# Performance work log

Hardware: AMD Instinct MI355X
Metric: run time of the kernel (lower is better)

## Reference

```python
import jax, jax.numpy as jnp
import numpy as np

N, L, H, K, T = 768, 8, 64, 4, 3

def _mlp2(x, w1, b1, w2, b2):
    # Linear -> ReLU -> Linear -> ReLU (matches nn.Sequential in q/k/v MLPs)
    return jax.nn.relu(jax.nn.relu(x @ w1 + b1) @ w2 + b2)

def setup_inputs() -> dict:
    key = jax.random.key(0)
    ks = jax.random.split(key, 20)
    s = 1.0 / np.sqrt(H)
    def lin(k, din, dout):
        return jax.random.uniform(k, (din, dout), jnp.float32, -s, s)
    def bias(k, dout):
        return jax.random.uniform(k, (dout,), jnp.float32, -s, s)
    inp = {
        "h": jax.random.normal(ks[0], (N, L, H), jnp.float32),
        "coord": jax.random.normal(ks[1], (N, L, K, T), jnp.float32),
        "wq1": lin(ks[2], H, H), "bq1": bias(ks[3], H),
        "wq2": lin(ks[4], H, H), "bq2": bias(ks[5], H),
        "wk1": lin(ks[6], H, H), "bk1": bias(ks[7], H),
        "wk2": lin(ks[8], H, H), "bk2": bias(ks[9], H),
        "wv1": lin(ks[10], H, H), "bv1": bias(ks[11], H),
        "wv2": lin(ks[12], H, H), "bv2": bias(ks[13], H),
        "wc1": lin(ks[14], H, H), "bc1": bias(ks[15], H),
        # final coord layer: Linear(H, 4, bias=False), xavier gain=0.001
        "wc2": jax.random.normal(ks[16], (H, K), jnp.float32) * 0.001,
    }
    return inp

def reference(h, coord, wq1, bq1, wq2, bq2, wk1, bk1, wk2, bk2,
              wv1, bv1, wv2, bv2, wc1, bc1, wc2):
    q = _mlp2(h, wq1, bq1, wq2, bq2)          # [N, L, H]
    k = _mlp2(h, wk1, bk1, wk2, bk2)          # [N, L, H]
    v = _mlp2(h, wv1, bv1, wv2, bv2)          # [N, L, H]
    # scores[i, j, l] = <q_i, k_j> per frame l; softmax over neighbor axis j (dim=1)
    scores = jnp.einsum('ilh,jlh->ijl', q, k)
    alpha = jax.nn.softmax(scores, axis=1)     # [N, N, L]
    h_agg = jnp.einsum('ijl,jlh->ilh', alpha, v)
    cmv = jax.nn.relu(v @ wc1 + bc1) @ wc2     # coord_mlp(v): [N, L, 4]
    coord_diff = coord[:, None] - coord[None]  # [N, N, L, 4, 3]
    x_agg = jnp.einsum('ijlkt,ijl,jlk->ilkt', coord_diff, alpha, cmv)
    return (h + h_agg, coord + x_agg)
```

## Files before the change

### kernel.cpp

```cpp
#include <hip/hip_runtime.h>
#include <hip/hip_bf16.h>

#define NN 768
#define LL 8
#define HH 64
#define IT 16
#define ABP 776
#define XST 80
#define WST 72

typedef __attribute__((ext_vector_type(8))) short bf16x8;
typedef __attribute__((ext_vector_type(4))) float f32x4;

__device__ __forceinline__ short f2bf(float x) {
    union { __hip_bfloat16 h; short s; } u;
    u.h = __float2bfloat16(x);
    return u.s;
}

__device__ __forceinline__ bf16x8 pack8(float4 lo, float4 hi) {
    bf16x8 r;
    r[0] = f2bf(lo.x); r[1] = f2bf(lo.y); r[2] = f2bf(lo.z); r[3] = f2bf(lo.w);
    r[4] = f2bf(hi.x); r[5] = f2bf(hi.y); r[6] = f2bf(hi.z); r[7] = f2bf(hi.w);
    return r;
}

__device__ __forceinline__ void stage_W(short (*Wt)[WST],
                                        const float* __restrict__ W, int t) {
    const int n  = t & 63;
    const int kb = (t >> 6) * 16;
    #pragma unroll
    for (int jj = 0; jj < 16; ++jj)
        Wt[n][kb + jj] = f2bf(W[(kb + jj) * 64 + n]);
}

__device__ __forceinline__ void layer_mfma_lds(bf16x8 a0, bf16x8 a1,
                                               const short (*Wt)[WST],
                                               const float* __restrict__ bias,
                                               int m, int quad, bool do_relu,
                                               f32x4 dout[4])
{
    #pragma unroll
    for (int nt = 0; nt < 4; ++nt) {
        const int n = nt * 16 + m;
        bf16x8 b0 = *(const bf16x8*)&Wt[n][quad * 8];
        bf16x8 b1 = *(const bf16x8*)&Wt[n][32 + quad * 8];
        f32x4 d = {0.f, 0.f, 0.f, 0.f};
        d = __builtin_amdgcn_mfma_f32_16x16x32_bf16(a0, b0, d, 0, 0, 0);
        d = __builtin_amdgcn_mfma_f32_16x16x32_bf16(a1, b1, d, 0, 0, 0);
        if (bias) {
            const float bb = bias[n];
            #pragma unroll
            for (int rg = 0; rg < 4; ++rg) d[rg] += bb;
        }
        if (do_relu) {
            #pragma unroll
            for (int rg = 0; rg < 4; ++rg) d[rg] = fmaxf(d[rg], 0.f);
        }
        dout[nt] = d;
    }
}

__device__ __forceinline__ void d_to_X(const f32x4 d[4], short (*X)[XST],
                                       int m, int quad) {
    #pragma unroll
    for (int nt = 0; nt < 4; ++nt)
        #pragma unroll
        for (int rg = 0; rg < 4; ++rg)
            X[quad * 4 + rg][nt * 16 + m] = f2bf(d[nt][rg]);
}

__global__ __launch_bounds__(256) void qkv_kernel(
    const float* __restrict__ h, const float* __restrict__ coord,
    const float* __restrict__ wq1, const float* __restrict__ bq1,
    const float* __restrict__ wq2, const float* __restrict__ bq2,
    const float* __restrict__ wk1, const float* __restrict__ bk1,
    const float* __restrict__ wk2, const float* __restrict__ bk2,
    const float* __restrict__ wv1, const float* __restrict__ bv1,
    const float* __restrict__ wv2, const float* __restrict__ bv2,
    const float* __restrict__ wc1, const float* __restrict__ bc1,
    const float* __restrict__ wc2,
    short* __restrict__ q_ws, short* __restrict__ k_ws,
    short* __restrict__ vT_ws, short* __restrict__ UT_ws)
{
    const int t    = threadIdx.x;
    const int lane = t & 63;
    const int w    = t >> 6;

    const int bb = blockIdx.x;
    int chain, tb;
    if (bb < 96)       { chain = 2; tb = bb; }
    else if (bb < 192) { chain = 0; tb = bb - 96; }
    else               { chain = 1; tb = bb - 192; }
    const int rt = tb * 4 + w;
    const int r0 = rt * 16;

    const int m    = lane & 15;
    const int quad = lane >> 4;

    __shared__ alignas(16) short Wt[3][64][WST];
    __shared__ alignas(16) short Xs[4][16][XST];
    __shared__ float cms[4][16][4];
    short (*X)[XST] = Xs[w];

    bf16x8 a0, a1;
    {
        const float* hrow = h + (size_t)(r0 + m) * 64;
        a0 = pack8(*(const float4*)(hrow + quad * 8),
                   *(const float4*)(hrow + quad * 8 + 4));
        a1 = pack8(*(const float4*)(hrow + 32 + quad * 8),
                   *(const float4*)(hrow + 32 + quad * 8 + 4));
    }

    float cpre[3];
    const int rowu = lane >> 2, kk = lane & 3;
    const int gu = r0 + rowu;
    if (chain == 2) {
        #pragma unroll
        for (int s = 0; s < 3; ++s)
            cpre[s] = coord[gu * 12 + kk * 3 + s];
    }

    if (chain == 0)      { stage_W(Wt[0], wq1, t); stage_W(Wt[1], wq2, t); }
    else if (chain == 1) { stage_W(Wt[0], wk1, t); stage_W(Wt[1], wk2, t); }
    else                 { stage_W(Wt[0], wv1, t); stage_W(Wt[1], wv2, t);
                           stage_W(Wt[2], wc1, t); }
    __syncthreads();

    f32x4 d[4];

    if (chain == 0) {
        layer_mfma_lds(a0, a1, Wt[0], bq1, m, quad, true, d);
        d_to_X(d, X, m, quad);
        __builtin_amdgcn_wave_barrier();
        a0 = *(const bf16x8*)&X[m][quad * 8];
        a1 = *(const bf16x8*)&X[m][32 + quad * 8];
        layer_mfma_lds(a0, a1, Wt[1], bq2, m, quad, true, d);
        #pragma unroll
        for (int nt = 0; nt < 4; ++nt)
            #pragma unroll
            for (int rg = 0; rg < 4; ++rg) {
                const int g = r0 + quad * 4 + rg, i = g >> 3, l = g & 7;
                q_ws[(l * NN + i) * 64 + nt * 16 + m] = f2bf(d[nt][rg]);
            }
    } else if (chain == 1) {
        layer_mfma_lds(a0, a1, Wt[0], bk1, m, quad, true, d);
        d_to_X(d, X, m, quad);
        __builtin_amdgcn_wave_barrier();
        a0 = *(const bf16x8*)&X[m][quad * 8];
        a1 = *(const bf16x8*)&X[m][32 + quad * 8];
        layer_mfma_lds(a0, a1, Wt[1], bk2, m, quad, true, d);
        #pragma unroll
        for (int nt = 0; nt < 4; ++nt)
            #pragma unroll
            for (int rg = 0; rg < 4; ++rg) {
                const int g = r0 + quad * 4 + rg, i = g >> 3, l = g & 7;
                k_ws[(l * NN + i) * 64 + nt * 16 + m] = f2bf(d[nt][rg]);
            }
    } else {
        layer_mfma_lds(a0, a1, Wt[0], bv1, m, quad, true, d);
        d_to_X(d, X, m, quad);
        __builtin_amdgcn_wave_barrier();
        a0 = *(const bf16x8*)&X[m][quad * 8];
        a1 = *(const bf16x8*)&X[m][32 + quad * 8];
        layer_mfma_lds(a0, a1, Wt[1], bv2, m, quad, true, d);
        #pragma unroll
        for (int nt = 0; nt < 4; ++nt)
            #pragma unroll
            for (int rg = 0; rg < 4; ++rg) {
                const int g = r0 + quad * 4 + rg, i = g >> 3, l = g & 7;
                vT_ws[((size_t)l * 64 + nt * 16 + m) * NN + i] = f2bf(d[nt][rg]);
            }
        d_to_X(d, X, m, quad);
        __builtin_amdgcn_wave_barrier();
        a0 = *(const bf16x8*)&X[m][quad * 8];
        a1 = *(const bf16x8*)&X[m][32 + quad * 8];
        layer_mfma_lds(a0, a1, Wt[2], bc1, m, quad, true, d);
        d_to_X(d, X, m, quad);
        __builtin_amdgcn_wave_barrier();
        a0 = *(const bf16x8*)&X[m][quad * 8];
        a1 = *(const bf16x8*)&X[m][32 + quad * 8];
        {
            bf16x8 b0, b1;
            #pragma unroll
            for (int j = 0; j < 8; ++j) {
                b0[j] = (m < 4) ? f2bf(wc2[(quad * 8 + j) * 4 + m]) : (short)0;
                b1[j] = (m < 4) ? f2bf(wc2[(32 + quad * 8 + j) * 4 + m]) : (short)0;
            }
            f32x4 dc = {0.f, 0.f, 0.f, 0.f};
            dc = __builtin_amdgcn_mfma_f32_16x16x32_bf16(a0, b0, dc, 0, 0, 0);
            dc = __builtin_amdgcn_mfma_f32_16x16x32_bf16(a1, b1, dc, 0, 0, 0);
            if (m < 4) {
                #pragma unroll
                for (int rg = 0; rg < 4; ++rg)
                    cms[w][quad * 4 + rg][m] = dc[rg];
            }
        }
        __builtin_amdgcn_wave_barrier();
        {
            const float c = cms[w][rowu][kk];
            const int i = gu >> 3, l = gu & 7;
            UT_ws[((size_t)l * 16 + kk * 4 + 0) * NN + i] = f2bf(c);
            #pragma unroll
            for (int seg = 1; seg < 4; ++seg) {
                const float uval = c * cpre[seg - 1];
                UT_ws[((size_t)l * 16 + kk * 4 + seg) * NN + i] = f2bf(uval);
            }
        }
    }
}

__global__ __launch_bounds__(256, 2) void attn_kernel(
    const short* __restrict__ q_ws, const short* __restrict__ k_ws,
    const short* __restrict__ vT_ws, const short* __restrict__ UT_ws,
    const float* __restrict__ h, const float* __restrict__ coord,
    float* __restrict__ h_out, float* __restrict__ x_out)
{
    const int l    = blockIdx.x & 7;
    const int i0   = (blockIdx.x >> 3) * IT;
    const int t    = threadIdx.x;
    const int lane = t & 63;
    const int w    = t >> 6;
    const int m    = lane & 15;
    const int quad = lane >> 4;

    __shared__ alignas(16) short al[IT][ABP];
    __shared__ float wmax[4][IT];
    __shared__ float wsum[4][IT];
    __shared__ float part3[4][IT][16];

    const int c = 16 * w + m;
    float hpre[4];
    #pragma unroll
    for (int rg = 0; rg < 4; ++rg)
        hpre[rg] = h[((i0 + quad * 4 + rg) * 8 + l) * 64 + c];
    float cdpre = 0.f;
    if (t < 192)
        cdpre = coord[((i0 + t / 12) * 8 + l) * 12 + (t % 12)];

    const bf16x8 aq0 = *(const bf16x8*)&q_ws[((size_t)l * NN + i0 + m) * 64 + quad * 8];
    const bf16x8 aq1 = *(const bf16x8*)&q_ws[((size_t)l * NN + i0 + m) * 64 + 32 + quad * 8];

    f32x4 dsc[12];
    {
        const short* kl = k_ws + (size_t)l * NN * 64;
        #pragma unroll
        for (int nt = 0; nt < 12; ++nt) {
            const int jb = 192 * w + nt * 16;
            const short* krow = kl + (size_t)(jb + m) * 64;
            bf16x8 b0 = *(const bf16x8*)(krow + quad * 8);
            bf16x8 b1 = *(const bf16x8*)(krow + 32 + quad * 8);
            f32x4 d = {0.f, 0.f, 0.f, 0.f};
            d = __builtin_amdgcn_mfma_f32_16x16x32_bf16(aq0, b0, d, 0, 0, 0);
            d = __builtin_amdgcn_mfma_f32_16x16x32_bf16(aq1, b1, d, 0, 0, 0);
            dsc[nt] = d;
        }
    }

    float mx[4];
    #pragma unroll
    for (int rg = 0; rg < 4; ++rg) {
        float mm = dsc[0][rg];
        #pragma unroll
        for (int nt = 1; nt < 12; ++nt) mm = fmaxf(mm, dsc[nt][rg]);
        mm = fmaxf(mm, __shfl_xor(mm, 1, 64));
        mm = fmaxf(mm, __shfl_xor(mm, 2, 64));
        mm = fmaxf(mm, __shfl_xor(mm, 4, 64));
        mm = fmaxf(mm, __shfl_xor(mm, 8, 64));
        if (m == 0) wmax[w][quad * 4 + rg] = mm;
    }
    __syncthreads();
    #pragma unroll
    for (int rg = 0; rg < 4; ++rg) {
        const int row = quad * 4 + rg;
        mx[rg] = fmaxf(fmaxf(wmax[0][row], wmax[1][row]),
                       fmaxf(wmax[2][row], wmax[3][row]));
    }

    const short* vrow = vT_ws + ((size_t)l * 64 + 16 * w + m) * NN;
    const short* urow = UT_ws + ((size_t)l * 16 + m) * NN + 192 * w;
    bf16x8 vpre[24];
    bf16x8 upre[6];
    #pragma unroll
    for (int kt = 0; kt < 24; ++kt)
        vpre[kt] = *(const bf16x8*)(vrow + kt * 32 + quad * 8);
    #pragma unroll
    for (int kt = 0; kt < 6; ++kt)
        upre[kt] = *(const bf16x8*)(urow + kt * 32 + quad * 8);

    float sl[4] = {0.f, 0.f, 0.f, 0.f};
    #pragma unroll
    for (int nt = 0; nt < 12; ++nt) {
        const int jb = 192 * w + nt * 16;
        #pragma unroll
        for (int rg = 0; rg < 4; ++rg) {
            const float e = __expf(dsc[nt][rg] - mx[rg]);
            sl[rg] += e;
            al[quad * 4 + rg][jb + m] = f2bf(e);
        }
    }
    #pragma unroll
    for (int rg = 0; rg < 4; ++rg) {
        float s = sl[rg];
        s += __shfl_xor(s, 1, 64);
        s += __shfl_xor(s, 2, 64);
        s += __shfl_xor(s, 4, 64);
        s += __shfl_xor(s, 8, 64);
        if (m == 0) wsum[w][quad * 4 + rg] = s;
    }
    __syncthreads();

    {
        f32x4 acc0 = {0.f, 0.f, 0.f, 0.f};
        f32x4 acc1 = {0.f, 0.f, 0.f, 0.f};
        #pragma unroll
        for (int kt = 0; kt < 24; kt += 2) {
            const int ka = kt * 32, kb = ka + 32;
            bf16x8 a0 = *(const bf16x8*)&al[m][ka + quad * 8];
            bf16x8 a1 = *(const bf16x8*)&al[m][kb + quad * 8];
            acc0 = __builtin_amdgcn_mfma_f32_16x16x32_bf16(a0, vpre[kt], acc0, 0, 0, 0);
            acc1 = __builtin_amdgcn_mfma_f32_16x16x32_bf16(a1, vpre[kt + 1], acc1, 0, 0, 0);
        }
        #pragma unroll
        for (int rg = 0; rg < 4; ++rg) {
            const int i = quad * 4 + rg;
            const float ri = 1.f / (wsum[0][i] + wsum[1][i] +
                                    wsum[2][i] + wsum[3][i]);
            const int row = ((i0 + i) * 8 + l) * 64 + c;
            h_out[row] = hpre[rg] + ri * (acc0[rg] + acc1[rg]);
        }
    }

    {
        f32x4 acc = {0.f, 0.f, 0.f, 0.f};
        #pragma unroll
        for (int kt = 0; kt < 6; ++kt) {
            const int k0 = kt * 32;
            bf16x8 a = *(const bf16x8*)&al[m][192 * w + k0 + quad * 8];
            acc = __builtin_amdgcn_mfma_f32_16x16x32_bf16(a, upre[kt], acc, 0, 0, 0);
        }
        #pragma unroll
        for (int rg = 0; rg < 4; ++rg)
            part3[w][quad * 4 + rg][m] = acc[rg];
    }
    __syncthreads();
    if (t < 192) {
        const int i4 = t / 12, kt = t % 12, k4 = kt / 3, s4 = kt % 3;
        const float ri = 1.f / (wsum[0][i4] + wsum[1][i4] +
                                wsum[2][i4] + wsum[3][i4]);
        const int uA = k4 * 4, uB = k4 * 4 + 1 + s4;
        const float sA = (part3[0][i4][uA] + part3[1][i4][uA] +
                          part3[2][i4][uA] + part3[3][i4][uA]) * ri;
        const float sB = (part3[0][i4][uB] + part3[1][i4][uB] +
                          part3[2][i4][uB] + part3[3][i4][uB]) * ri;
        const int idx = ((i0 + i4) * 8 + l) * 12 + kt;
        x_out[idx] = cdpre + cdpre * sA - sB;
    }
}

extern "C" void kernel_launch(void* const* d_in, const int* in_sizes, int n_in,
                              void* d_out, int out_size, void* d_ws, size_t ws_size,
                              hipStream_t stream) {
    const float* h     = (const float*)d_in[0];
    const float* coord = (const float*)d_in[1];

    float* h_out = (float*)d_out;
    float* x_out = h_out + NN * LL * HH;

    short* q_ws  = (short*)d_ws;
    short* k_ws  = q_ws + NN * LL * HH;
    short* vT_ws = k_ws + NN * LL * HH;
    short* UT_ws = vT_ws + NN * LL * HH;

    qkv_kernel<<<288, 256, 0, stream>>>(
        h, coord,
        (const float*)d_in[2],  (const float*)d_in[3],
        (const float*)d_in[4],  (const float*)d_in[5],
        (const float*)d_in[6],  (const float*)d_in[7],
        (const float*)d_in[8],  (const float*)d_in[9],
        (const float*)d_in[10], (const float*)d_in[11],
        (const float*)d_in[12], (const float*)d_in[13],
        (const float*)d_in[14], (const float*)d_in[15],
        (const float*)d_in[16],
        q_ws, k_ws, vT_ws, UT_ws);

    attn_kernel<<<(NN / IT) * LL, 256, 0, stream>>>(
        q_ws, k_ws, vT_ws, UT_ws, h, coord, h_out, x_out);
}
```

Measured before the change: 110.2 us.

## Fuse QKV and attention kernels into one persistent launch with grid barrier

Merges the QKV projection kernel and the attention kernel into a single 384-block launch. A software grid-wide barrier (an atomic counter in workspace, reset by a memset each call) sits between the projection phase and the attention phase. Shared memory is overlaid with a union, and the h/coord prefetch is hoisted ahead of the barrier. This removes one kernel launch and its inter-kernel gap. In exchange it adds a memset, spin-wait overhead, and a deadlock risk if all 384 blocks are not co-resident.

```diff
diff --git a/kernel.cpp b/kernel.cpp
--- a/kernel.cpp
+++ b/kernel.cpp
@@ -8,6 +8,7 @@
 #define ABP 776
 #define XST 80
 #define WST 72
+#define GRID 384
 
 typedef __attribute__((ext_vector_type(8))) short bf16x8;
 typedef __attribute__((ext_vector_type(4))) float f32x4;
@@ -70,7 +71,35 @@
             X[quad * 4 + rg][nt * 16 + m] = f2bf(d[nt][rg]);
 }
 
-__global__ __launch_bounds__(256) void qkv_kernel(
+union SMem {
+    struct {
+        short Wt[3][64][WST];
+        short Xs[4][16][XST];
+        float cms[4][16][4];
+    } q;
+    struct {
+        short al[IT][ABP];
+        float wmax[4][IT];
+        float wsum[4][IT];
+        float part3[4][IT][16];
+    } a;
+};
+
+__device__ __forceinline__ void grid_barrier(unsigned* cnt) {
+    __threadfence();
+    __syncthreads();
+    if (threadIdx.x == 0) {
+        __hip_atomic_fetch_add(cnt, 1u, __ATOMIC_RELEASE,
+                               __HIP_MEMORY_SCOPE_AGENT);
+        while (__hip_atomic_load(cnt, __ATOMIC_ACQUIRE,
+                                 __HIP_MEMORY_SCOPE_AGENT) < GRID)
+            __builtin_amdgcn_s_sleep(1);
+    }
+    __syncthreads();
+    __threadfence();
+}
+
+__global__ __launch_bounds__(256, 2) void fused_kernel(
     const float* __restrict__ h, const float* __restrict__ coord,
     const float* __restrict__ wq1, const float* __restrict__ bq1,
     const float* __restrict__ wq2, const float* __restrict__ bq2,
@@ -81,169 +110,155 @@
     const float* __restrict__ wc1, const float* __restrict__ bc1,
     const float* __restrict__ wc2,
     short* __restrict__ q_ws, short* __restrict__ k_ws,
-    short* __restrict__ vT_ws, short* __restrict__ UT_ws)
+    short* __restrict__ vT_ws, short* __restrict__ UT_ws,
+    float* __restrict__ h_out, float* __restrict__ x_out,
+    unsigned* __restrict__ bar)
 {
-    const int t    = threadIdx.x;
-    const int lane = t & 63;
-    const int w    = t >> 6;
-
-    const int bb = blockIdx.x;
-    int chain, tb;
-    if (bb < 96)       { chain = 2; tb = bb; }
-    else if (bb < 192) { chain = 0; tb = bb - 96; }
-    else               { chain = 1; tb = bb - 192; }
-    const int rt = tb * 4 + w;
-    const int r0 = rt * 16;
-
-    const int m    = lane & 15;
-    const int quad = lane >> 4;
-
-    __shared__ alignas(16) short Wt[3][64][WST];
-    __shared__ alignas(16) short Xs[4][16][XST];
-    __shared__ float cms[4][16][4];
-    short (*X)[XST] = Xs[w];
-
-    bf16x8 a0, a1;
-    {
-        const float* hrow = h + (size_t)(r0 + m) * 64;
-        a0 = pack8(*(const float4*)(hrow + quad * 8),
-                   *(const float4*)(hrow + quad * 8 + 4));
-        a1 = pack8(*(const float4*)(hrow + 32 + quad * 8),
-                   *(const float4*)(hrow + 32 + quad * 8 + 4));
-    }
-
-    float cpre[3];
-    const int rowu = lane >> 2, kk = lane & 3;
-    const int gu = r0 + rowu;
-    if (chain == 2) {
-        #pragma unroll
-        for (int s = 0; s < 3; ++s)
-            cpre[s] = coord[gu * 12 + kk * 3 + s];
-    }
-
-    if (chain == 0)      { stage_W(Wt[0], wq1, t); stage_W(Wt[1], wq2, t); }
-    else if (chain == 1) { stage_W(Wt[0], wk1, t); stage_W(Wt[1], wk2, t); }
-    else                 { stage_W(Wt[0], wv1, t); stage_W(Wt[1], wv2, t);
-                           stage_W(Wt[2], wc1, t); }
-    __syncthreads();
-
-    f32x4 d[4];
-
-    if (chain == 0) {
-        layer_mfma_lds(a0, a1, Wt[0], bq1, m, quad, true, d);
-        d_to_X(d, X, m, quad);
-        __builtin_amdgcn_wave_barrier();
-        a0 = *(const bf16x8*)&X[m][quad * 8];
-        a1 = *(const bf16x8*)&X[m][32 + quad * 8];
-        layer_mfma_lds(a0, a1, Wt[1], bq2, m, quad, true, d);
-        #pragma unroll
-        for (int nt = 0; nt < 4; ++nt)
-            #pragma unroll
-            for (int rg = 0; rg < 4; ++rg) {
-                const int g = r0 + quad * 4 + rg, i = g >> 3, l = g & 7;
-                q_ws[(l * NN + i) * 64 + nt * 16 + m] = f2bf(d[nt][rg]);
-            }
-    } else if (chain == 1) {
-        layer_mfma_lds(a0, a1, Wt[0], bk1, m, quad, true, d);
-        d_to_X(d, X, m, quad);
-        __builtin_amdgcn_wave_barrier();
-        a0 = *(const bf16x8*)&X[m][quad * 8];
-        a1 = *(const bf16x8*)&X[m][32 + quad * 8];
-        layer_mfma_lds(a0, a1, Wt[1], bk2, m, quad, true, d);
-        #pragma unroll
-        for (int nt = 0; nt < 4; ++nt)
-            #pragma unroll
-            for (int rg = 0; rg < 4; ++rg) {
-                const int g = r0 + quad * 4 + rg, i = g >> 3, l = g & 7;
-                k_ws[(l * NN + i) * 64 + nt * 16 + m] = f2bf(d[nt][rg]);
-            }
-    } else {
-        layer_mfma_lds(a0, a1, Wt[0], bv1, m, quad, true, d);
-        d_to_X(d, X, m, quad);
-        __builtin_amdgcn_wave_barrier();
-        a0 = *(const bf16x8*)&X[m][quad * 8];
-        a1 = *(const bf16x8*)&X[m][32 + quad * 8];
-        layer_mfma_lds(a0, a1, Wt[1], bv2, m, quad, true, d);
-        #pragma unroll
-        for (int nt = 0; nt < 4; ++nt)
-            #pragma unroll
-            for (int rg = 0; rg < 4; ++rg) {
-                const int g = r0 + quad * 4 + rg, i = g >> 3, l = g & 7;
-                vT_ws[((size_t)l * 64 + nt * 16 + m) * NN + i] = f2bf(d[nt][rg]);
-            }
-        d_to_X(d, X, m, quad);
-        __builtin_amdgcn_wave_barrier();
-        a0 = *(const bf16x8*)&X[m][quad * 8];
-        a1 = *(const bf16x8*)&X[m][32 + quad * 8];
-        layer_mfma_lds(a0, a1, Wt[2], bc1, m, quad, true, d);
-        d_to_X(d, X, m, quad);
-        __builtin_amdgcn_wave_barrier();
-        a0 = *(const bf16x8*)&X[m][quad * 8];
-        a1 = *(const bf16x8*)&X[m][32 + quad * 8];
-        {
-            bf16x8 b0, b1;
-            #pragma unroll
-            for (int j = 0; j < 8; ++j) {
-                b0[j] = (m < 4) ? f2bf(wc2[(quad * 8 + j) * 4 + m]) : (short)0;
-                b1[j] = (m < 4) ? f2bf(wc2[(32 + quad * 8 + j) * 4 + m]) : (short)0;
-            }
-            f32x4 dc = {0.f, 0.f, 0.f, 0.f};
-            dc = __builtin_amdgcn_mfma_f32_16x16x32_bf16(a0, b0, dc, 0, 0, 0);
-            dc = __builtin_amdgcn_mfma_f32_16x16x32_bf16(a1, b1, dc, 0, 0, 0);
-            if (m < 4) {
-                #pragma unroll
-                for (int rg = 0; rg < 4; ++rg)
-                    cms[w][quad * 4 + rg][m] = dc[rg];
-            }
-        }
-        __builtin_amdgcn_wave_barrier();
-        {
-            const float c = cms[w][rowu][kk];
-            const int i = gu >> 3, l = gu & 7;
-            UT_ws[((size_t)l * 16 + kk * 4 + 0) * NN + i] = f2bf(c);
-            #pragma unroll
-            for (int seg = 1; seg < 4; ++seg) {
-                const float uval = c * cpre[seg - 1];
-                UT_ws[((size_t)l * 16 + kk * 4 + seg) * NN + i] = f2bf(uval);
-            }
-        }
-    }
-}
-
-__global__ __launch_bounds__(256, 2) void attn_kernel(
-    const short* __restrict__ q_ws, const short* __restrict__ k_ws,
-    const short* __restrict__ vT_ws, const short* __restrict__ UT_ws,
-    const float* __restrict__ h, const float* __restrict__ coord,
-    float* __restrict__ h_out, float* __restrict__ x_out)
-{
-    const int l    = blockIdx.x & 7;
-    const int i0   = (blockIdx.x >> 3) * IT;
+    const int bb   = blockIdx.x;
     const int t    = threadIdx.x;
     const int lane = t & 63;
     const int w    = t >> 6;
     const int m    = lane & 15;
     const int quad = lane >> 4;
 
-    __shared__ alignas(16) short al[IT][ABP];
-    __shared__ float wmax[4][IT];
-    __shared__ float wsum[4][IT];
-    __shared__ float part3[4][IT][16];
-
-    const int c = 16 * w + m;
+    __shared__ SMem sm;
+
+    const int l2 = bb & 7;
+    const int i0 = (bb >> 3) * IT;
+    const int c  = 16 * w + m;
     float hpre[4];
     #pragma unroll
     for (int rg = 0; rg < 4; ++rg)
-        hpre[rg] = h[((i0 + quad * 4 + rg) * 8 + l) * 64 + c];
+        hpre[rg] = h[((i0 + quad * 4 + rg) * 8 + l2) * 64 + c];
     float cdpre = 0.f;
     if (t < 192)
-        cdpre = coord[((i0 + t / 12) * 8 + l) * 12 + (t % 12)];
-
-    const bf16x8 aq0 = *(const bf16x8*)&q_ws[((size_t)l * NN + i0 + m) * 64 + quad * 8];
-    const bf16x8 aq1 = *(const bf16x8*)&q_ws[((size_t)l * NN + i0 + m) * 64 + 32 + quad * 8];
+        cdpre = coord[((i0 + t / 12) * 8 + l2) * 12 + (t % 12)];
+
+    if (bb < 288) {
+        int chain, tb;
+        if (bb < 96)       { chain = 2; tb = bb; }
+        else if (bb < 192) { chain = 0; tb = bb - 96; }
+        else               { chain = 1; tb = bb - 192; }
+        const int rt = tb * 4 + w;
+        const int r0 = rt * 16;
+
+        short (*X)[XST] = sm.q.Xs[w];
+
+        bf16x8 a0, a1;
+        {
+            const float* hrow = h + (size_t)(r0 + m) * 64;
+            a0 = pack8(*(const float4*)(hrow + quad * 8),
+                       *(const float4*)(hrow + quad * 8 + 4));
+            a1 = pack8(*(const float4*)(hrow + 32 + quad * 8),
+                       *(const float4*)(hrow + 32 + quad * 8 + 4));
+        }
+
+        float cpre[3];
+        const int rowu = lane >> 2, kk = lane & 3;
+        const int gu = r0 + rowu;
+        if (chain == 2) {
+            #pragma unroll
+            for (int s = 0; s < 3; ++s)
+                cpre[s] = coord[gu * 12 + kk * 3 + s];
+        }
+
+        if (chain == 0)      { stage_W(sm.q.Wt[0], wq1, t); stage_W(sm.q.Wt[1], wq2, t); }
+        else if (chain == 1) { stage_W(sm.q.Wt[0], wk1, t); stage_W(sm.q.Wt[1], wk2, t); }
+        else                 { stage_W(sm.q.Wt[0], wv1, t); stage_W(sm.q.Wt[1], wv2, t);
+                               stage_W(sm.q.Wt[2], wc1, t); }
+        __syncthreads();
+
+        f32x4 d[4];
+
+        if (chain == 0) {
+            layer_mfma_lds(a0, a1, sm.q.Wt[0], bq1, m, quad, true, d);
+            d_to_X(d, X, m, quad);
+            __builtin_amdgcn_wave_barrier();
+            a0 = *(const bf16x8*)&X[m][quad * 8];
+            a1 = *(const bf16x8*)&X[m][32 + quad * 8];
+            layer_mfma_lds(a0, a1, sm.q.Wt[1], bq2, m, quad, true, d);
+            #pragma unroll
+            for (int nt = 0; nt < 4; ++nt)
+                #pragma unroll
+                for (int rg = 0; rg < 4; ++rg) {
+                    const int g = r0 + quad * 4 + rg, i = g >> 3, l = g & 7;
+                    q_ws[(l * NN + i) * 64 + nt * 16 + m] = f2bf(d[nt][rg]);
+                }
+        } else if (chain == 1) {
+            layer_mfma_lds(a0, a1, sm.q.Wt[0], bk1, m, quad, true, d);
+            d_to_X(d, X, m, quad);
+            __builtin_amdgcn_wave_barrier();
+            a0 = *(const bf16x8*)&X[m][quad * 8];
+            a1 = *(const bf16x8*)&X[m][32 + quad * 8];
+            layer_mfma_lds(a0, a1, sm.q.Wt[1], bk2, m, quad, true, d);
+            #pragma unroll
+            for (int nt = 0; nt < 4; ++nt)
+                #pragma unroll
+                for (int rg = 0; rg < 4; ++rg) {
+                    const int g = r0 + quad * 4 + rg, i = g >> 3, l = g & 7;
+                    k_ws[(l * NN + i) * 64 + nt * 16 + m] = f2bf(d[nt][rg]);
+                }
+        } else {
+            layer_mfma_lds(a0, a1, sm.q.Wt[0], bv1, m, quad, true, d);
+            d_to_X(d, X, m, quad);
+            __builtin_amdgcn_wave_barrier();
+            a0 = *(const bf16x8*)&X[m][quad * 8];
+            a1 = *(const bf16x8*)&X[m][32 + quad * 8];
+            layer_mfma_lds(a0, a1, sm.q.Wt[1], bv2, m, quad, true, d);
+            #pragma unroll
+            for (int nt = 0; nt < 4; ++nt)
+                #pragma unroll
+                for (int rg = 0; rg < 4; ++rg) {
+                    const int g = r0 + quad * 4 + rg, i = g >> 3, l = g & 7;
+                    vT_ws[((size_t)l * 64 + nt * 16 + m) * NN + i] = f2bf(d[nt][rg]);
+                }
+            d_to_X(d, X, m, quad);
+            __builtin_amdgcn_wave_barrier();
+            a0 = *(const bf16x8*)&X[m][quad * 8];
+            a1 = *(const bf16x8*)&X[m][32 + quad * 8];
+            layer_mfma_lds(a0, a1, sm.q.Wt[2], bc1, m, quad, true, d);
+            d_to_X(d, X, m, quad);
+            __builtin_amdgcn_wave_barrier();
+            a0 = *(const bf16x8*)&X[m][quad * 8];
+            a1 = *(const bf16x8*)&X[m][32 + quad * 8];
+            {
+                bf16x8 b0, b1;
+                #pragma unroll
+                for (int j = 0; j < 8; ++j) {
+                    b0[j] = (m < 4) ? f2bf(wc2[(quad * 8 + j) * 4 + m]) : (short)0;
+                    b1[j] = (m < 4) ? f2bf(wc2[(32 + quad * 8 + j) * 4 + m]) : (short)0;
+                }
+                f32x4 dc = {0.f, 0.f, 0.f, 0.f};
+                dc = __builtin_amdgcn_mfma_f32_16x16x32_bf16(a0, b0, dc, 0, 0, 0);
+                dc = __builtin_amdgcn_mfma_f32_16x16x32_bf16(a1, b1, dc, 0, 0, 0);
+                if (m < 4) {
+                    #pragma unroll
+                    for (int rg = 0; rg < 4; ++rg)
+                        sm.q.cms[w][quad * 4 + rg][m] = dc[rg];
+                }
+            }
+            __builtin_amdgcn_wave_barrier();
+            {
+                const float cv = sm.q.cms[w][rowu][kk];
+                const int i = gu >> 3, l = gu & 7;
+                UT_ws[((size_t)l * 16 + kk * 4 + 0) * NN + i] = f2bf(cv);
+                #pragma unroll
+                for (int seg = 1; seg < 4; ++seg) {
+                    const float uval = cv * cpre[seg - 1];
+                    UT_ws[((size_t)l * 16 + kk * 4 + seg) * NN + i] = f2bf(uval);
+                }
+            }
+        }
+    }
+
+    grid_barrier(bar);
+
+    const bf16x8 aq0 = *(const bf16x8*)&q_ws[((size_t)l2 * NN + i0 + m) * 64 + quad * 8];
+    const bf16x8 aq1 = *(const bf16x8*)&q_ws[((size_t)l2 * NN + i0 + m) * 64 + 32 + quad * 8];
 
     f32x4 dsc[12];
     {
-        const short* kl = k_ws + (size_t)l * NN * 64;
+        const short* kl = k_ws + (size_t)l2 * NN * 64;
         #pragma unroll
         for (int nt = 0; nt < 12; ++nt) {
             const int jb = 192 * w + nt * 16;
@@ -267,18 +282,18 @@
         mm = fmaxf(mm, __shfl_xor(mm, 2, 64));
         mm = fmaxf(mm, __shfl_xor(mm, 4, 64));
         mm = fmaxf(mm, __shfl_xor(mm, 8, 64));
-        if (m == 0) wmax[w][quad * 4 + rg] = mm;
+        if (m == 0) sm.a.wmax[w][quad * 4 + rg] = mm;
     }
     __syncthreads();
     #pragma unroll
     for (int rg = 0; rg < 4; ++rg) {
         const int row = quad * 4 + rg;
-        mx[rg] = fmaxf(fmaxf(wmax[0][row], wmax[1][row]),
-                       fmaxf(wmax[2][row], wmax[3][row]));
-    }
-
-    const short* vrow = vT_ws + ((size_t)l * 64 + 16 * w + m) * NN;
-    const short* urow = UT_ws + ((size_t)l * 16 + m) * NN + 192 * w;
+        mx[rg] = fmaxf(fmaxf(sm.a.wmax[0][row], sm.a.wmax[1][row]),
+                       fmaxf(sm.a.wmax[2][row], sm.a.wmax[3][row]));
+    }
+
+    const short* vrow = vT_ws + ((size_t)l2 * 64 + 16 * w + m) * NN;
+    const short* urow = UT_ws + ((size_t)l2 * 16 + m) * NN + 192 * w;
     bf16x8 vpre[24];
     bf16x8 upre[6];
     #pragma unroll
@@ -296,7 +311,7 @@
         for (int rg = 0; rg < 4; ++rg) {
             const float e = __expf(dsc[nt][rg] - mx[rg]);
             sl[rg] += e;
-            al[quad * 4 + rg][jb + m] = f2bf(e);
+            sm.a.al[quad * 4 + rg][jb + m] = f2bf(e);
         }
     }
     #pragma unroll
@@ -306,7 +321,7 @@
         s += __shfl_xor(s, 2, 64);
         s += __shfl_xor(s, 4, 64);
         s += __shfl_xor(s, 8, 64);
-        if (m == 0) wsum[w][quad * 4 + rg] = s;
+        if (m == 0) sm.a.wsum[w][quad * 4 + rg] = s;
     }
     __syncthreads();
 
@@ -316,17 +331,17 @@
         #pragma unroll
         for (int kt = 0; kt < 24; kt += 2) {
             const int ka = kt * 32, kb = ka + 32;
-            bf16x8 a0 = *(const bf16x8*)&al[m][ka + quad * 8];
-            bf16x8 a1 = *(const bf16x8*)&al[m][kb + quad * 8];
+            bf16x8 a0 = *(const bf16x8*)&sm.a.al[m][ka + quad * 8];
+            bf16x8 a1 = *(const bf16x8*)&sm.a.al[m][kb + quad * 8];
             acc0 = __builtin_amdgcn_mfma_f32_16x16x32_bf16(a0, vpre[kt], acc0, 0, 0, 0);
             acc1 = __builtin_amdgcn_mfma_f32_16x16x32_bf16(a1, vpre[kt + 1], acc1, 0, 0, 0);
         }
         #pragma unroll
         for (int rg = 0; rg < 4; ++rg) {
             const int i = quad * 4 + rg;
-            const float ri = 1.f / (wsum[0][i] + wsum[1][i] +
-                                    wsum[2][i] + wsum[3][i]);
-            const int row = ((i0 + i) * 8 + l) * 64 + c;
+            const float ri = 1.f / (sm.a.wsum[0][i] + sm.a.wsum[1][i] +
+                                    sm.a.wsum[2][i] + sm.a.wsum[3][i]);
+            const int row = ((i0 + i) * 8 + l2) * 64 + c;
             h_out[row] = hpre[rg] + ri * (acc0[rg] + acc1[rg]);
         }
     }
@@ -336,24 +351,24 @@
         #pragma unroll
         for (int kt = 0; kt < 6; ++kt) {
             const int k0 = kt * 32;
-            bf16x8 a = *(const bf16x8*)&al[m][192 * w + k0 + quad * 8];
+            bf16x8 a = *(const bf16x8*)&sm.a.al[m][192 * w + k0 + quad * 8];
             acc = __builtin_amdgcn_mfma_f32_16x16x32_bf16(a, upre[kt], acc, 0, 0, 0);
         }
         #pragma unroll
         for (int rg = 0; rg < 4; ++rg)
-            part3[w][quad * 4 + rg][m] = acc[rg];
+            sm.a.part3[w][quad * 4 + rg][m] = acc[rg];
     }
     __syncthreads();
     if (t < 192) {
         const int i4 = t / 12, kt = t % 12, k4 = kt / 3, s4 = kt % 3;
-        const float ri = 1.f / (wsum[0][i4] + wsum[1][i4] +
-                                wsum[2][i4] + wsum[3][i4]);
+        const float ri = 1.f / (sm.a.wsum[0][i4] + sm.a.wsum[1][i4] +
+                                sm.a.wsum[2][i4] + sm.a.wsum[3][i4]);
         const int uA = k4 * 4, uB = k4 * 4 + 1 + s4;
-        const float sA = (part3[0][i4][uA] + part3[1][i4][uA] +
-                          part3[2][i4][uA] + part3[3][i4][uA]) * ri;
-        const float sB = (part3[0][i4][uB] + part3[1][i4][uB] +
-                          part3[2][i4][uB] + part3[3][i4][uB]) * ri;
-        const int idx = ((i0 + i4) * 8 + l) * 12 + kt;
+        const float sA = (sm.a.part3[0][i4][uA] + sm.a.part3[1][i4][uA] +
+                          sm.a.part3[2][i4][uA] + sm.a.part3[3][i4][uA]) * ri;
+        const float sB = (sm.a.part3[0][i4][uB] + sm.a.part3[1][i4][uB] +
+                          sm.a.part3[2][i4][uB] + sm.a.part3[3][i4][uB]) * ri;
+        const int idx = ((i0 + i4) * 8 + l2) * 12 + kt;
         x_out[idx] = cdpre + cdpre * sA - sB;
     }
 }
@@ -372,7 +387,10 @@
     short* vT_ws = k_ws + NN * LL * HH;
     short* UT_ws = vT_ws + NN * LL * HH;
 
-    qkv_kernel<<<288, 256, 0, stream>>>(
+    unsigned* bar = (unsigned*)((char*)d_ws + ws_size - 256);
+    hipMemsetAsync((void*)bar, 0, 256, stream);
+
+    fused_kernel<<<GRID, 256, 0, stream>>>(
         h, coord,
         (const float*)d_in[2],  (const float*)d_in[3],
         (const float*)d_in[4],  (const float*)d_in[5],
@@ -382,8 +400,5 @@
         (const float*)d_in[12], (const float*)d_in[13],
         (const float*)d_in[14], (const float*)d_in[15],
         (const float*)d_in[16],
-        q_ws, k_ws, vT_ws, UT_ws);
-
-    attn_kernel<<<(NN / IT) * LL, 256, 0, stream>>>(
-        q_ws, k_ws, vT_ws, UT_ws, h, coord, h_out, x_out);
-}
+        q_ws, k_ws, vT_ws, UT_ws, h_out, x_out, bar);
+}
```

After: 275.1 us. 150% more time.

## Fuse query MLP into attention kernel and drop q workspace round-trip

Applied to the files above, without the earlier changes.

Moves the two-layer Q MLP out of the projection kernel into the attention kernel. Each attention block stages wq1/wq2 in shared memory and computes its 16 query rows with MFMA. Shared memory for this is overlaid with the attention buffers through a union. This removes the q_ws global write and read and shrinks the first kernel from 288 to 192 blocks. In exchange, every attention block redoes weight staging and the MLP, which all four waves compute redundantly.

```diff
diff --git a/kernel.cpp b/kernel.cpp
--- a/kernel.cpp
+++ b/kernel.cpp
@@ -70,30 +70,26 @@
             X[quad * 4 + rg][nt * 16 + m] = f2bf(d[nt][rg]);
 }
 
-__global__ __launch_bounds__(256) void qkv_kernel(
+__global__ __launch_bounds__(256) void kv_kernel(
     const float* __restrict__ h, const float* __restrict__ coord,
-    const float* __restrict__ wq1, const float* __restrict__ bq1,
-    const float* __restrict__ wq2, const float* __restrict__ bq2,
     const float* __restrict__ wk1, const float* __restrict__ bk1,
     const float* __restrict__ wk2, const float* __restrict__ bk2,
     const float* __restrict__ wv1, const float* __restrict__ bv1,
     const float* __restrict__ wv2, const float* __restrict__ bv2,
     const float* __restrict__ wc1, const float* __restrict__ bc1,
     const float* __restrict__ wc2,
-    short* __restrict__ q_ws, short* __restrict__ k_ws,
-    short* __restrict__ vT_ws, short* __restrict__ UT_ws)
+    short* __restrict__ k_ws, short* __restrict__ vT_ws,
+    short* __restrict__ UT_ws)
 {
     const int t    = threadIdx.x;
     const int lane = t & 63;
     const int w    = t >> 6;
 
-    const int bb = blockIdx.x;
-    int chain, tb;
-    if (bb < 96)       { chain = 2; tb = bb; }
-    else if (bb < 192) { chain = 0; tb = bb - 96; }
-    else               { chain = 1; tb = bb - 192; }
-    const int rt = tb * 4 + w;
-    const int r0 = rt * 16;
+    const int bb    = blockIdx.x;
+    const int chain = (bb < 96) ? 2 : 1;
+    const int tb    = (bb < 96) ? bb : bb - 96;
+    const int rt    = tb * 4 + w;
+    const int r0    = rt * 16;
 
     const int m    = lane & 15;
     const int quad = lane >> 4;
@@ -121,29 +117,14 @@
             cpre[s] = coord[gu * 12 + kk * 3 + s];
     }
 
-    if (chain == 0)      { stage_W(Wt[0], wq1, t); stage_W(Wt[1], wq2, t); }
-    else if (chain == 1) { stage_W(Wt[0], wk1, t); stage_W(Wt[1], wk2, t); }
-    else                 { stage_W(Wt[0], wv1, t); stage_W(Wt[1], wv2, t);
-                           stage_W(Wt[2], wc1, t); }
+    if (chain == 1) { stage_W(Wt[0], wk1, t); stage_W(Wt[1], wk2, t); }
+    else            { stage_W(Wt[0], wv1, t); stage_W(Wt[1], wv2, t);
+                      stage_W(Wt[2], wc1, t); }
     __syncthreads();
 
     f32x4 d[4];
 
-    if (chain == 0) {
-        layer_mfma_lds(a0, a1, Wt[0], bq1, m, quad, true, d);
-        d_to_X(d, X, m, quad);
-        __builtin_amdgcn_wave_barrier();
-        a0 = *(const bf16x8*)&X[m][quad * 8];
-        a1 = *(const bf16x8*)&X[m][32 + quad * 8];
-        layer_mfma_lds(a0, a1, Wt[1], bq2, m, quad, true, d);
-        #pragma unroll
-        for (int nt = 0; nt < 4; ++nt)
-            #pragma unroll
-            for (int rg = 0; rg < 4; ++rg) {
-                const int g = r0 + quad * 4 + rg, i = g >> 3, l = g & 7;
-                q_ws[(l * NN + i) * 64 + nt * 16 + m] = f2bf(d[nt][rg]);
-            }
-    } else if (chain == 1) {
+    if (chain == 1) {
         layer_mfma_lds(a0, a1, Wt[0], bk1, m, quad, true, d);
         d_to_X(d, X, m, quad);
         __builtin_amdgcn_wave_barrier();
@@ -198,22 +179,38 @@
         }
         __builtin_amdgcn_wave_barrier();
         {
-            const float c = cms[w][rowu][kk];
+            const float cv = cms[w][rowu][kk];
             const int i = gu >> 3, l = gu & 7;
-            UT_ws[((size_t)l * 16 + kk * 4 + 0) * NN + i] = f2bf(c);
+            UT_ws[((size_t)l * 16 + kk * 4 + 0) * NN + i] = f2bf(cv);
             #pragma unroll
             for (int seg = 1; seg < 4; ++seg) {
-                const float uval = c * cpre[seg - 1];
+                const float uval = cv * cpre[seg - 1];
                 UT_ws[((size_t)l * 16 + kk * 4 + seg) * NN + i] = f2bf(uval);
             }
         }
     }
 }
 
+union SMemA {
+    struct {
+        short Wt[2][64][WST];
+        short X1[16][XST];
+        short X2[16][XST];
+    } qp;
+    struct {
+        short al[IT][ABP];
+        float wmax[4][IT];
+        float wsum[4][IT];
+        float part3[4][IT][16];
+    } a;
+};
+
 __global__ __launch_bounds__(256, 2) void attn_kernel(
-    const short* __restrict__ q_ws, const short* __restrict__ k_ws,
-    const short* __restrict__ vT_ws, const short* __restrict__ UT_ws,
+    const short* __restrict__ k_ws, const short* __restrict__ vT_ws,
+    const short* __restrict__ UT_ws,
     const float* __restrict__ h, const float* __restrict__ coord,
+    const float* __restrict__ wq1, const float* __restrict__ bq1,
+    const float* __restrict__ wq2, const float* __restrict__ bq2,
     float* __restrict__ h_out, float* __restrict__ x_out)
 {
     const int l    = blockIdx.x & 7;
@@ -224,10 +221,7 @@
     const int m    = lane & 15;
     const int quad = lane >> 4;
 
-    __shared__ alignas(16) short al[IT][ABP];
-    __shared__ float wmax[4][IT];
-    __shared__ float wsum[4][IT];
-    __shared__ float part3[4][IT][16];
+    __shared__ SMemA sm;
 
     const int c = 16 * w + m;
     float hpre[4];
@@ -238,8 +232,30 @@
     if (t < 192)
         cdpre = coord[((i0 + t / 12) * 8 + l) * 12 + (t % 12)];
 
-    const bf16x8 aq0 = *(const bf16x8*)&q_ws[((size_t)l * NN + i0 + m) * 64 + quad * 8];
-    const bf16x8 aq1 = *(const bf16x8*)&q_ws[((size_t)l * NN + i0 + m) * 64 + 32 + quad * 8];
+    stage_W(sm.qp.Wt[0], wq1, t);
+    stage_W(sm.qp.Wt[1], wq2, t);
+    __syncthreads();
+
+    bf16x8 aq0, aq1;
+    {
+        bf16x8 a0, a1;
+        const float* hrow = h + ((size_t)(i0 + m) * 8 + l) * 64;
+        a0 = pack8(*(const float4*)(hrow + quad * 8),
+                   *(const float4*)(hrow + quad * 8 + 4));
+        a1 = pack8(*(const float4*)(hrow + 32 + quad * 8),
+                   *(const float4*)(hrow + 32 + quad * 8 + 4));
+        f32x4 d[4];
+        layer_mfma_lds(a0, a1, sm.qp.Wt[0], bq1, m, quad, true, d);
+        d_to_X(d, sm.qp.X1, m, quad);
+        __builtin_amdgcn_wave_barrier();
+        a0 = *(const bf16x8*)&sm.qp.X1[m][quad * 8];
+        a1 = *(const bf16x8*)&sm.qp.X1[m][32 + quad * 8];
+        layer_mfma_lds(a0, a1, sm.qp.Wt[1], bq2, m, quad, true, d);
+        d_to_X(d, sm.qp.X2, m, quad);
+        __builtin_amdgcn_wave_barrier();
+        aq0 = *(const bf16x8*)&sm.qp.X2[m][quad * 8];
+        aq1 = *(const bf16x8*)&sm.qp.X2[m][32 + quad * 8];
+    }
 
     f32x4 dsc[12];
     {
@@ -267,14 +283,14 @@
         mm = fmaxf(mm, __shfl_xor(mm, 2, 64));
         mm = fmaxf(mm, __shfl_xor(mm, 4, 64));
         mm = fmaxf(mm, __shfl_xor(mm, 8, 64));
-        if (m == 0) wmax[w][quad * 4 + rg] = mm;
+        if (m == 0) sm.a.wmax[w][quad * 4 + rg] = mm;
     }
     __syncthreads();
     #pragma unroll
     for (int rg = 0; rg < 4; ++rg) {
         const int row = quad * 4 + rg;
-        mx[rg] = fmaxf(fmaxf(wmax[0][row], wmax[1][row]),
-                       fmaxf(wmax[2][row], wmax[3][row]));
+        mx[rg] = fmaxf(fmaxf(sm.a.wmax[0][row], sm.a.wmax[1][row]),
+                       fmaxf(sm.a.wmax[2][row], sm.a.wmax[3][row]));
     }
 
     const short* vrow = vT_ws + ((size_t)l * 64 + 16 * w + m) * NN;
@@ -296,7 +312,7 @@
         for (int rg = 0; rg < 4; ++rg) {
             const float e = __expf(dsc[nt][rg] - mx[rg]);
             sl[rg] += e;
-            al[quad * 4 + rg][jb + m] = f2bf(e);
+            sm.a.al[quad * 4 + rg][jb + m] = f2bf(e);
         }
     }
     #pragma unroll
@@ -306,7 +322,7 @@
         s += __shfl_xor(s, 2, 64);
         s += __shfl_xor(s, 4, 64);
         s += __shfl_xor(s, 8, 64);
-        if (m == 0) wsum[w][quad * 4 + rg] = s;
+        if (m == 0) sm.a.wsum[w][quad * 4 + rg] = s;
     }
     __syncthreads();
 
@@ -316,16 +332,16 @@
         #pragma unroll
         for (int kt = 0; kt < 24; kt += 2) {
             const int ka = kt * 32, kb = ka + 32;
-            bf16x8 a0 = *(const bf16x8*)&al[m][ka + quad * 8];
-            bf16x8 a1 = *(const bf16x8*)&al[m][kb + quad * 8];
+            bf16x8 a0 = *(const bf16x8*)&sm.a.al[m][ka + quad * 8];
+            bf16x8 a1 = *(const bf16x8*)&sm.a.al[m][kb + quad * 8];
             acc0 = __builtin_amdgcn_mfma_f32_16x16x32_bf16(a0, vpre[kt], acc0, 0, 0, 0);
             acc1 = __builtin_amdgcn_mfma_f32_16x16x32_bf16(a1, vpre[kt + 1], acc1, 0, 0, 0);
         }
         #pragma unroll
         for (int rg = 0; rg < 4; ++rg) {
             const int i = quad * 4 + rg;
-            const float ri = 1.f / (wsum[0][i] + wsum[1][i] +
-                                    wsum[2][i] + wsum[3][i]);
+            const float ri = 1.f / (sm.a.wsum[0][i] + sm.a.wsum[1][i] +
+                                    sm.a.wsum[2][i] + sm.a.wsum[3][i]);
             const int row = ((i0 + i) * 8 + l) * 64 + c;
             h_out[row] = hpre[rg] + ri * (acc0[rg] + acc1[rg]);
         }
@@ -336,23 +352,23 @@
         #pragma unroll
         for (int kt = 0; kt < 6; ++kt) {
             const int k0 = kt * 32;
-            bf16x8 a = *(const bf16x8*)&al[m][192 * w + k0 + quad * 8];
+            bf16x8 a = *(const bf16x8*)&sm.a.al[m][192 * w + k0 + quad * 8];
             acc = __builtin_amdgcn_mfma_f32_16x16x32_bf16(a, upre[kt], acc, 0, 0, 0);
         }
         #pragma unroll
         for (int rg = 0; rg < 4; ++rg)
-            part3[w][quad * 4 + rg][m] = acc[rg];
+            sm.a.part3[w][quad * 4 + rg][m] = acc[rg];
     }
     __syncthreads();
     if (t < 192) {
         const int i4 = t / 12, kt = t % 12, k4 = kt / 3, s4 = kt % 3;
-        const float ri = 1.f / (wsum[0][i4] + wsum[1][i4] +
-                                wsum[2][i4] + wsum[3][i4]);
+        const float ri = 1.f / (sm.a.wsum[0][i4] + sm.a.wsum[1][i4] +
+                                sm.a.wsum[2][i4] + sm.a.wsum[3][i4]);
         const int uA = k4 * 4, uB = k4 * 4 + 1 + s4;
-        const float sA = (part3[0][i4][uA] + part3[1][i4][uA] +
-                          part3[2][i4][uA] + part3[3][i4][uA]) * ri;
-        const float sB = (part3[0][i4][uB] + part3[1][i4][uB] +
-                          part3[2][i4][uB] + part3[3][i4][uB]) * ri;
+        const float sA = (sm.a.part3[0][i4][uA] + sm.a.part3[1][i4][uA] +
+                          sm.a.part3[2][i4][uA] + sm.a.part3[3][i4][uA]) * ri;
+        const float sB = (sm.a.part3[0][i4][uB] + sm.a.part3[1][i4][uB] +
+                          sm.a.part3[2][i4][uB] + sm.a.part3[3][i4][uB]) * ri;
         const int idx = ((i0 + i4) * 8 + l) * 12 + kt;
         x_out[idx] = cdpre + cdpre * sA - sB;
     }
@@ -372,18 +388,19 @@
     short* vT_ws = k_ws + NN * LL * HH;
     short* UT_ws = vT_ws + NN * LL * HH;
 
-    qkv_kernel<<<288, 256, 0, stream>>>(
+    kv_kernel<<<192, 256, 0, stream>>>(
         h, coord,
-        (const float*)d_in[2],  (const float*)d_in[3],
-        (const float*)d_in[4],  (const float*)d_in[5],
         (const float*)d_in[6],  (const float*)d_in[7],
         (const float*)d_in[8],  (const float*)d_in[9],
         (const float*)d_in[10], (const float*)d_in[11],
         (const float*)d_in[12], (const float*)d_in[13],
         (const float*)d_in[14], (const float*)d_in[15],
         (const float*)d_in[16],
-        q_ws, k_ws, vT_ws, UT_ws);
+        k_ws, vT_ws, UT_ws);
 
     attn_kernel<<<(NN / IT) * LL, 256, 0, stream>>>(
-        q_ws, k_ws, vT_ws, UT_ws, h, coord, h_out, x_out);
-}
+        k_ws, vT_ws, UT_ws, h, coord,
+        (const float*)d_in[2], (const float*)d_in[3],
+        (const float*)d_in[4], (const float*)d_in[5],
+        h_out, x_out);
+}
```

Measured after the change: 115.4 us. 1.05x slower.
